# Optimization experiments

Hardware: AMD Instinct MI355X
Metric: run time of the kernel (lower is better)

## Reference

```python
import jax, jax.numpy as jnp
import numpy as np


def setup_inputs() -> dict:
    key = jax.random.key(0)
    ks = jax.random.split(key, 6)
    B, H, T, Dk, Dv = 64, 16, 4, 128, 256
    q = jax.random.normal(ks[0], (B, H, T, Dk), dtype=jnp.float32)
    k = jax.random.normal(ks[1], (B, H, T, Dk), dtype=jnp.float32)
    v = jax.random.normal(ks[2], (B, H, T, Dv), dtype=jnp.float32)
    g = jax.random.uniform(ks[3], (B, H, T), dtype=jnp.float32)
    beta = jax.random.uniform(ks[4], (B, H, T), dtype=jnp.float32)
    last_recurrent_state = jax.random.normal(ks[5], (B, H, Dk, Dv), dtype=jnp.float32)
    return {"q": q, "k": k, "v": v, "g": g, "beta": beta,
            "last_recurrent_state": last_recurrent_state}


def reference(q, k, v, g, beta, last_recurrent_state):
    # q,k: (B,H,T,Dk)  v: (B,H,T,Dv)  g,beta: (B,H,T)  state: (B,H,Dk,Dv)
    def step(state, xs):
        q_t, k_t, v_t, g_t, beta_t = xs  # (B,H,Dk),(B,H,Dk),(B,H,Dv),(B,H),(B,H)
        state = state * jnp.exp(g_t)[..., None, None]           # decay
        kv_mem = jnp.einsum('bhkv,bhk->bhv', state, k_t)         # readout with key
        delta = (v_t - kv_mem) * beta_t[..., None]               # delta-rule correction
        state = state + k_t[..., None] * delta[..., None, :]     # rank-1 update
        out_t = jnp.einsum('bhkv,bhk->bhv', state, q_t)          # query readout
        return state, out_t

    xs = (jnp.moveaxis(q, 2, 0), jnp.moveaxis(k, 2, 0), jnp.moveaxis(v, 2, 0),
          jnp.moveaxis(g, 2, 0), jnp.moveaxis(beta, 2, 0))
    state, outs = jax.lax.scan(step, last_recurrent_state, xs)
    output = jnp.moveaxis(outs, 0, 2)  # (B,H,T,Dv)
    return jnp.concatenate([output.reshape(-1), state.reshape(-1)], axis=0)
```

## Files before the change

kernel.cpp:

```cpp
#include <hip/hip_runtime.h>

#define BH   1024
#define TT   4
#define DK   128
#define DV   256

__global__ __launch_bounds__(256)
void delta_rule_kernel(const float* __restrict__ q,
                       const float* __restrict__ k,
                       const float* __restrict__ v,
                       const float* __restrict__ g,
                       const float* __restrict__ beta,
                       const float* __restrict__ s0,
                       float* __restrict__ out)
{
    const int bh   = blockIdx.x;
    const int vcol = threadIdx.x;

    const float* __restrict__ sin_p = s0 + (size_t)bh * DK * DV;
    float* __restrict__ out_p  = out + (size_t)bh * TT * DV;
    float* __restrict__ sout_p = out + (size_t)BH * TT * DV + (size_t)bh * DK * DV;

    const float* __restrict__ kbase = k    + (size_t)bh * TT * DK;
    const float* __restrict__ qbase = q    + (size_t)bh * TT * DK;
    const float* __restrict__ vbase = v    + (size_t)bh * TT * DV;
    const float* __restrict__ gbase = g    + (size_t)bh * TT;
    const float* __restrict__ bbase = beta + (size_t)bh * TT;

    float s[DK];
#pragma unroll
    for (int kk = 0; kk < DK; ++kk)
        s[kk] = sin_p[(size_t)kk * DV + vcol];

    __shared__ float kq[2 * DK];

    for (int t = 0; t < TT; ++t) {
        __syncthreads();
        if (vcol < DK) kq[vcol]      = kbase[t * DK + vcol];
        else           kq[vcol]      = qbase[t * DK + (vcol - DK)];
        __syncthreads();

        const float gt = expf(gbase[t]);
        const float bt = bbase[t];
        const float vt = vbase[t * DV + vcol];

        float kv = 0.0f;
#pragma unroll
        for (int kk = 0; kk < DK; ++kk) {
            s[kk] *= gt;
            kv = fmaf(s[kk], kq[kk], kv);
        }

        const float delta = (vt - kv) * bt;

        float o = 0.0f;
#pragma unroll
        for (int kk = 0; kk < DK; ++kk) {
            s[kk] = fmaf(kq[kk], delta, s[kk]);
            o = fmaf(s[kk], kq[DK + kk], o);
        }

        out_p[t * DV + vcol] = o;
    }

#pragma unroll
    for (int kk = 0; kk < DK; ++kk)
        sout_p[(size_t)kk * DV + vcol] = s[kk];
}

extern "C" void kernel_launch(void* const* d_in, const int* in_sizes, int n_in,
                              void* d_out, int out_size, void* d_ws, size_t ws_size,
                              hipStream_t stream) {
    const float* q    = (const float*)d_in[0];
    const float* k    = (const float*)d_in[1];
    const float* v    = (const float*)d_in[2];
    const float* g    = (const float*)d_in[3];
    const float* beta = (const float*)d_in[4];
    const float* s0   = (const float*)d_in[5];
    float* out = (float*)d_out;

    delta_rule_kernel<<<dim3(BH), dim3(256), 0, stream>>>(q, k, v, g, beta, s0, out);
}
```

Baseline: 289.4 us.

## Split Dk across lanes with shuffle reductions and float4 state tiles per thread

Each (b,h) is now split into two blocks over the value dimension. Each thread holds a 16x4 state tile: 16 key rows by 4 value columns, loaded and stored as float4. Partial dot products over the key dimension are reduced across 8 lanes with xor shuffles, and k and q are staged in padded shared memory. The aim is to cut per-thread register pressure from 128 floats to 64, allow wider memory accesses, and double the block count for better occupancy. The cost is extra shuffle reductions and strided float4 global accesses across key rows.

```diff
diff --git a/kernel.cpp b/kernel.cpp
--- a/kernel.cpp
+++ b/kernel.cpp
@@ -1,9 +1,13 @@
 #include <hip/hip_runtime.h>
 
-#define BH   1024
-#define TT   4
-#define DK   128
-#define DV   256
+#define BH    1024
+#define TT    4
+#define DK    128
+#define DV    256
+#define KSEG  8
+#define KLEN  16
+#define HALFV 128
+#define LDP   17
 
 __global__ __launch_bounds__(256)
 void delta_rule_kernel(const float* __restrict__ q,
@@ -14,8 +18,13 @@
                        const float* __restrict__ s0,
                        float* __restrict__ out)
 {
-    const int bh   = blockIdx.x;
-    const int vcol = threadIdx.x;
+    const int bh   = blockIdx.x >> 1;
+    const int half = blockIdx.x & 1;
+    const int tid  = threadIdx.x;
+    const int kg   = tid & (KSEG - 1);
+    const int vg   = tid >> 3;
+    const int vcol = half * HALFV + vg * 4;
+    const int kr0  = kg * KLEN;
 
     const float* __restrict__ sin_p = s0 + (size_t)bh * DK * DV;
     float* __restrict__ out_p  = out + (size_t)bh * TT * DV;
@@ -27,45 +36,80 @@
     const float* __restrict__ gbase = g    + (size_t)bh * TT;
     const float* __restrict__ bbase = beta + (size_t)bh * TT;
 
-    float s[DK];
+    float4 s4[KLEN];
 #pragma unroll
-    for (int kk = 0; kk < DK; ++kk)
-        s[kk] = sin_p[(size_t)kk * DV + vcol];
+    for (int kk = 0; kk < KLEN; ++kk)
+        s4[kk] = *(const float4*)&sin_p[(size_t)(kr0 + kk) * DV + vcol];
 
-    __shared__ float kq[2 * DK];
+    __shared__ float ks[KSEG * LDP];
+    __shared__ float qs[KSEG * LDP];
 
     for (int t = 0; t < TT; ++t) {
         __syncthreads();
-        if (vcol < DK) kq[vcol]      = kbase[t * DK + vcol];
-        else           kq[vcol]      = qbase[t * DK + (vcol - DK)];
+        if (tid < DK) {
+            ks[(tid >> 4) * LDP + (tid & 15)] = kbase[t * DK + tid];
+        } else {
+            int j = tid - DK;
+            qs[(j >> 4) * LDP + (j & 15)] = qbase[t * DK + j];
+        }
         __syncthreads();
 
         const float gt = expf(gbase[t]);
         const float bt = bbase[t];
-        const float vt = vbase[t * DV + vcol];
+        const float4 v4 = *(const float4*)&vbase[t * DV + vcol];
 
-        float kv = 0.0f;
+        float4 kv = make_float4(0.f, 0.f, 0.f, 0.f);
 #pragma unroll
-        for (int kk = 0; kk < DK; ++kk) {
-            s[kk] *= gt;
-            kv = fmaf(s[kk], kq[kk], kv);
+        for (int kk = 0; kk < KLEN; ++kk) {
+            const float kt = ks[kg * LDP + kk];
+            s4[kk].x *= gt; s4[kk].y *= gt; s4[kk].z *= gt; s4[kk].w *= gt;
+            kv.x = fmaf(s4[kk].x, kt, kv.x);
+            kv.y = fmaf(s4[kk].y, kt, kv.y);
+            kv.z = fmaf(s4[kk].z, kt, kv.z);
+            kv.w = fmaf(s4[kk].w, kt, kv.w);
+        }
+#pragma unroll
+        for (int m = 1; m < KSEG; m <<= 1) {
+            kv.x += __shfl_xor(kv.x, m);
+            kv.y += __shfl_xor(kv.y, m);
+            kv.z += __shfl_xor(kv.z, m);
+            kv.w += __shfl_xor(kv.w, m);
         }
 
-        const float delta = (vt - kv) * bt;
+        float4 d4;
+        d4.x = (v4.x - kv.x) * bt;
+        d4.y = (v4.y - kv.y) * bt;
+        d4.z = (v4.z - kv.z) * bt;
+        d4.w = (v4.w - kv.w) * bt;
 
-        float o = 0.0f;
+        float4 o4 = make_float4(0.f, 0.f, 0.f, 0.f);
 #pragma unroll
-        for (int kk = 0; kk < DK; ++kk) {
-            s[kk] = fmaf(kq[kk], delta, s[kk]);
-            o = fmaf(s[kk], kq[DK + kk], o);
+        for (int kk = 0; kk < KLEN; ++kk) {
+            const float kt = ks[kg * LDP + kk];
+            const float qt = qs[kg * LDP + kk];
+            s4[kk].x = fmaf(kt, d4.x, s4[kk].x);
+            s4[kk].y = fmaf(kt, d4.y, s4[kk].y);
+            s4[kk].z = fmaf(kt, d4.z, s4[kk].z);
+            s4[kk].w = fmaf(kt, d4.w, s4[kk].w);
+            o4.x = fmaf(s4[kk].x, qt, o4.x);
+            o4.y = fmaf(s4[kk].y, qt, o4.y);
+            o4.z = fmaf(s4[kk].z, qt, o4.z);
+            o4.w = fmaf(s4[kk].w, qt, o4.w);
         }
-
-        out_p[t * DV + vcol] = o;
+#pragma unroll
+        for (int m = 1; m < KSEG; m <<= 1) {
+            o4.x += __shfl_xor(o4.x, m);
+            o4.y += __shfl_xor(o4.y, m);
+            o4.z += __shfl_xor(o4.z, m);
+            o4.w += __shfl_xor(o4.w, m);
+        }
+        if (kg == 0)
+            *(float4*)&out_p[t * DV + vcol] = o4;
     }
 
 #pragma unroll
-    for (int kk = 0; kk < DK; ++kk)
-        sout_p[(size_t)kk * DV + vcol] = s[kk];
+    for (int kk = 0; kk < KLEN; ++kk)
+        *(float4*)&sout_p[(size_t)(kr0 + kk) * DV + vcol] = s4[kk];
 }
 
 extern "C" void kernel_launch(void* const* d_in, const int* in_sizes, int n_in,
@@ -79,5 +123,5 @@
     const float* s0   = (const float*)d_in[5];
     float* out = (float*)d_out;
 
-    delta_rule_kernel<<<dim3(BH), dim3(256), 0, stream>>>(q, k, v, g, beta, s0, out);
+    delta_rule_kernel<<<dim3(BH * 2), dim3(256), 0, stream>>>(q, k, v, g, beta, s0, out);
 }
```

Result: faster. 262.7 us (-9.2%).
